# Performance work log

Hardware: AMD Instinct MI355X
Metric: run time of the kernel (lower is better)

Reference implementation:

```python
import jax, jax.numpy as jnp
import numpy as np

N = 100000   # total nodes (batched graphs)
E = 800000   # random edges (self-loops appended -> E+N total)
G = 2000     # number of graphs in batch
H = 4        # heads per GAT layer
D = 64       # hidden_size (per-head out dim)
IN = 64      # in_feats
EXTRA = 8    # extra graph-level feats
HID = H * D  # 256


def setup_inputs() -> dict:
    key = jax.random.key(0)
    ks = jax.random.split(key, 24)
    s = 0.5  # init std used in the torch module
    feats_node = jax.random.normal(ks[0], (N, IN), jnp.float32)
    feats_graph = jax.random.normal(ks[1], (G, EXTRA), jnp.float32)
    # edges + self loops (DGL GATConv requires no zero-in-degree nodes)
    src = jnp.concatenate([jax.random.randint(ks[2], (E,), 0, N), jnp.arange(N)])
    dst = jnp.concatenate([jax.random.randint(ks[3], (E,), 0, N), jnp.arange(N)])
    node_gid = jnp.sort(jax.random.randint(ks[4], (N,), 0, G))
    # GAT layer 1
    W1 = jax.random.normal(ks[5], (IN, HID), jnp.float32) * s
    al1 = jax.random.normal(ks[6], (H, D), jnp.float32) * s
    ar1 = jax.random.normal(ks[7], (H, D), jnp.float32) * s
    b1 = jnp.zeros((HID,), jnp.float32)
    # GAT layer 2
    W2 = jax.random.normal(ks[8], (HID, HID), jnp.float32) * s
    al2 = jax.random.normal(ks[9], (H, D), jnp.float32) * s
    ar2 = jax.random.normal(ks[10], (H, D), jnp.float32) * s
    b2 = jnp.zeros((HID,), jnp.float32)
    # WeightedAverage readout score
    Ws = jax.random.normal(ks[11], (HID, 1), jnp.float32) * s
    bs = jnp.zeros((1,), jnp.float32)
    # MLP: 264 -> 128 -> 64 -> 1 with SELU
    Wm1 = jax.random.normal(ks[12], (HID + EXTRA, 2 * D), jnp.float32) * s
    bm1 = jnp.zeros((2 * D,), jnp.float32)
    Wm2 = jax.random.normal(ks[13], (2 * D, D), jnp.float32) * s
    bm2 = jnp.zeros((D,), jnp.float32)
    Wm3 = jax.random.normal(ks[14], (D, 1), jnp.float32) * s
    bm3 = jnp.zeros((1,), jnp.float32)
    return dict(feats_node=feats_node, feats_graph=feats_graph,
                W1=W1, al1=al1, ar1=ar1, b1=b1,
                W2=W2, al2=al2, ar2=ar2, b2=b2,
                Ws=Ws, bs=bs, Wm1=Wm1, bm1=bm1, Wm2=Wm2, bm2=bm2,
                Wm3=Wm3, bm3=bm3,
                src=src, dst=dst, node_gid=node_gid)


def gat_layer(x, W, al, ar, b, src, dst):
    # DGL GATConv: fc -> per-node attn projections -> edge leaky_relu ->
    # edge softmax over incoming edges -> weighted scatter-sum -> +bias
    f = (x @ W).reshape(N, H, D)                       # [N,H,D]
    el = jnp.einsum('nhd,hd->nh', f, al)               # [N,H]
    er = jnp.einsum('nhd,hd->nh', f, ar)               # [N,H]
    e = jax.nn.leaky_relu(el[src] + er[dst], 0.2)      # [E',H]
    m = jax.ops.segment_max(e, dst, num_segments=N)    # per-dst max
    e = jnp.exp(e - m[dst])
    denom = jax.ops.segment_sum(e, dst, num_segments=N)
    alpha = e / denom[dst]                             # edge softmax [E',H]
    out = jax.ops.segment_sum(alpha[:, :, None] * f[src], dst, num_segments=N)
    return out.reshape(N, HID) + b


def reference(feats_node, feats_graph, W1, al1, ar1, b1, W2, al2, ar2, b2,
              Ws, bs, Wm1, bm1, Wm2, bm2, Wm3, bm3, src, dst, node_gid):
    x = jax.nn.relu(gat_layer(feats_node, W1, al1, ar1, b1, src, dst))
    x = jax.nn.relu(gat_layer(x, W2, al2, ar2, b2, src, dst))
    # weighted-average readout per graph: sum(w*x)/sum(w)
    w = jax.nn.sigmoid(x @ Ws + bs)                    # [N,1]
    num = jax.ops.segment_sum(w * x, node_gid, num_segments=G)
    den = jax.ops.segment_sum(w, node_gid, num_segments=G)
    emb = num / jnp.where(den == 0, 1.0, den)          # [G,HID]
    h = jnp.concatenate([emb, feats_graph], axis=1)    # [G,HID+EXTRA]
    h = jax.nn.selu(h @ Wm1 + bm1)
    h = jax.nn.selu(h @ Wm2 + bm2)
    return h @ Wm3 + bm3                               # [G,1]
```

## Files before the change

### kernel.cpp

```cpp
#include <hip/hip_runtime.h>
#include <hip/hip_bf16.h>
#include <math.h>

#define NN     100000
#define GG     2000
#define HH     4
#define DD     64
#define HID    256
#define INF_   64
#define EXTRA  8

typedef unsigned short u16;
typedef __attribute__((ext_vector_type(8))) short bf16x8;
typedef __attribute__((ext_vector_type(4))) float f32x4;

__device__ __forceinline__ u16 f2bf(float f) {
    unsigned u = __float_as_uint(f);
    return (u16)((u + 0x7fffu + ((u >> 16) & 1u)) >> 16);
}
__device__ __forceinline__ float bf2f(u16 v) {
    return __uint_as_float(((unsigned)v) << 16);
}

__global__ __launch_bounds__(256) void wsplit_kernel(
    const float* __restrict__ W, u16* __restrict__ hi, u16* __restrict__ lo,
    int K, int lgK)
{
    int idx = blockIdx.x * 256 + threadIdx.x;
    if (idx >= 256 * K) return;
    int n = idx >> lgK, k = idx & (K - 1);
    float w = W[k * HID + n];
    u16 h = f2bf(w);
    hi[idx] = h;
    lo[idx] = f2bf(w - bf2f(h));
}

__global__ __launch_bounds__(256) void walprep_kernel(
    const float* __restrict__ W1, const float* __restrict__ al,
    const float* __restrict__ ar, float* __restrict__ wal, float* __restrict__ war)
{
    int tid = threadIdx.x;
    int d = tid >> 2, h = tid & 3;
    const float* wrow = W1 + d * HID + h * DD;
    const float* av = al + h * DD;
    const float* bv = ar + h * DD;
    float s1 = 0.f, s2 = 0.f;
    for (int c = 0; c < DD; ++c) { s1 += wrow[c] * av[c]; s2 += wrow[c] * bv[c]; }
    wal[d * 4 + h] = s1;
    war[d * 4 + h] = s2;
}

__global__ __launch_bounds__(256) void elr1_kernel(
    const float* __restrict__ feats, const float* __restrict__ wal,
    const float* __restrict__ war, float* __restrict__ el, float* __restrict__ er)
{
    int idx = blockIdx.x * 256 + threadIdx.x;
    if (idx >= NN * HH) return;
    int n = idx >> 2, h = idx & 3;
    const float* f = feats + (size_t)n * INF_;
    float s1 = 0.f, s2 = 0.f;
    #pragma unroll 4
    for (int d = 0; d < INF_; d += 4) {
        float4 fv = *reinterpret_cast<const float4*>(f + d);
        s1 += fv.x * wal[(d + 0) * 4 + h] + fv.y * wal[(d + 1) * 4 + h]
            + fv.z * wal[(d + 2) * 4 + h] + fv.w * wal[(d + 3) * 4 + h];
        s2 += fv.x * war[(d + 0) * 4 + h] + fv.y * war[(d + 1) * 4 + h]
            + fv.z * war[(d + 2) * 4 + h] + fv.w * war[(d + 3) * 4 + h];
    }
    el[idx] = s1;
    er[idx] = s2;
}

__device__ __forceinline__ float leaky02(float x) { return x > 0.f ? x : 0.2f * x; }

__global__ __launch_bounds__(256) void edge_softmax_kernel(
    const float* __restrict__ el, const float* __restrict__ er,
    const int* __restrict__ rowptr, const int* __restrict__ colsrc,
    float* __restrict__ w, float* __restrict__ invden)
{
    int idx = blockIdx.x * 256 + threadIdx.x;
    if (idx >= NN * HH) return;
    int t = idx >> 2, h = idx & 3;
    int beg = rowptr[t], end = rowptr[t + 1];
    float ert = er[idx];
    float m = -1e30f;
    for (int i = beg; i < end; ++i) {
        int s = colsrc[i];
        m = fmaxf(m, leaky02(el[s * 4 + h] + ert));
    }
    float den = 0.f;
    for (int i = beg; i < end; ++i) {
        int s = colsrc[i];
        float v = expf(leaky02(el[s * 4 + h] + ert) - m);
        w[(size_t)i * 4 + h] = v;
        den += v;
    }
    invden[idx] = 1.f / den;
}

__global__ __launch_bounds__(256) void aggregate_feats_kernel(
    const float* __restrict__ feats, const float* __restrict__ w,
    const float* __restrict__ invden, const int* __restrict__ rowptr,
    const int* __restrict__ colsrc, u16* __restrict__ Yh, u16* __restrict__ Yl)
{
    int t = blockIdx.x * 4 + (threadIdx.x >> 6);
    int lane = threadIdx.x & 63;
    if (t >= NN) return;
    int beg = rowptr[t], end = rowptr[t + 1];
    float a0 = 0.f, a1 = 0.f, a2 = 0.f, a3 = 0.f;
    float b0 = 0.f, b1 = 0.f, b2 = 0.f, b3 = 0.f;
    int i = beg;
    for (; i + 1 < end; i += 2) {
        int s0 = colsrc[i], s1 = colsrc[i + 1];
        float4 w0 = *reinterpret_cast<const float4*>(w + (size_t)i * 4);
        float4 w1 = *reinterpret_cast<const float4*>(w + (size_t)(i + 1) * 4);
        float f0 = feats[(size_t)s0 * INF_ + lane];
        float f1 = feats[(size_t)s1 * INF_ + lane];
        a0 += w0.x * f0; a1 += w0.y * f0; a2 += w0.z * f0; a3 += w0.w * f0;
        b0 += w1.x * f1; b1 += w1.y * f1; b2 += w1.z * f1; b3 += w1.w * f1;
    }
    if (i < end) {
        int s0 = colsrc[i];
        float4 w0 = *reinterpret_cast<const float4*>(w + (size_t)i * 4);
        float f0 = feats[(size_t)s0 * INF_ + lane];
        a0 += w0.x * f0; a1 += w0.y * f0; a2 += w0.z * f0; a3 += w0.w * f0;
    }
    float4 inv = *reinterpret_cast<const float4*>(invden + (size_t)t * 4);
    float y0 = (a0 + b0) * inv.x;
    float y1 = (a1 + b1) * inv.y;
    float y2 = (a2 + b2) * inv.z;
    float y3 = (a3 + b3) * inv.w;
    u16* yh = Yh + (size_t)t * HID;
    u16* yl = Yl + (size_t)t * HID;
    u16 h0 = f2bf(y0), h1 = f2bf(y1), h2 = f2bf(y2), h3 = f2bf(y3);
    yh[lane] = h0;        yl[lane] = f2bf(y0 - bf2f(h0));
    yh[64 + lane] = h1;   yl[64 + lane] = f2bf(y1 - bf2f(h1));
    yh[128 + lane] = h2;  yl[128 + lane] = f2bf(y2 - bf2f(h2));
    yh[192 + lane] = h3;  yl[192 + lane] = f2bf(y3 - bf2f(h3));
}

__global__ __launch_bounds__(256) void gemm_head_kernel(
    const u16* __restrict__ Yh, const u16* __restrict__ Yl,
    const u16* __restrict__ BThi, const u16* __restrict__ BTlo,
    const float* __restrict__ bias,
    u16* __restrict__ Xh, u16* __restrict__ Xl, int M)
{
    __shared__ __align__(16) u16 Ah[128 * 64];
    __shared__ __align__(16) u16 Al[128 * 64];
    __shared__ __align__(16) u16 Bh[64 * 64];
    __shared__ __align__(16) u16 Bl[64 * 64];
    const int tid  = threadIdx.x;
    const int wave = tid >> 6, lane = tid & 63;
    const int quad = lane >> 4, l15 = lane & 15;
    const int wy = wave >> 1, wx = wave & 1;
    const int head = blockIdx.y;
    const int r0 = blockIdx.x * 128;
    const int cb = head * DD;

    {
        int row = tid >> 1, half = tid & 1;
        int gr = min(r0 + row, M - 1);
        size_t goff = (size_t)gr * HID + cb;
        #pragma unroll
        for (int m = 0; m < 4; ++m) {
            int c = half * 4 + m;
            int cs = c ^ (row & 7);
            *reinterpret_cast<bf16x8*>(&Ah[row * 64 + cs * 8]) =
                *reinterpret_cast<const bf16x8*>(Yh + goff + c * 8);
            *reinterpret_cast<bf16x8*>(&Al[row * 64 + cs * 8]) =
                *reinterpret_cast<const bf16x8*>(Yl + goff + c * 8);
        }
        int d = tid & 63, seg = tid >> 6;
        size_t boff = (size_t)(head * DD + d) * 64;
        #pragma unroll
        for (int m = 0; m < 2; ++m) {
            int c = seg * 2 + m;
            int cs = c ^ (d & 7);
            *reinterpret_cast<bf16x8*>(&Bh[d * 64 + cs * 8]) =
                *reinterpret_cast<const bf16x8*>(BThi + boff + c * 8);
            *reinterpret_cast<bf16x8*>(&Bl[d * 64 + cs * 8]) =
                *reinterpret_cast<const bf16x8*>(BTlo + boff + c * 8);
        }
    }
    __syncthreads();

    f32x4 acc[4][2];
    #pragma unroll
    for (int i = 0; i < 4; ++i)
        #pragma unroll
        for (int j = 0; j < 2; ++j)
            acc[i][j] = (f32x4){0.f, 0.f, 0.f, 0.f};

    #pragma unroll
    for (int k0 = 0; k0 < 64; k0 += 32) {
        bf16x8 afh[4], afl[4], bfh[2], bfl[2];
        #pragma unroll
        for (int i = 0; i < 4; ++i) {
            int Ra = wy * 64 + i * 16 + l15;
            int c = (k0 >> 3) + quad;
            int cs = c ^ (Ra & 7);
            afh[i] = *reinterpret_cast<const bf16x8*>(&Ah[Ra * 64 + cs * 8]);
            afl[i] = *reinterpret_cast<const bf16x8*>(&Al[Ra * 64 + cs * 8]);
        }
        #pragma unroll
        for (int j = 0; j < 2; ++j) {
            int Rb = wx * 32 + j * 16 + l15;
            int c = (k0 >> 3) + quad;
            int cs = c ^ (Rb & 7);
            bfh[j] = *reinterpret_cast<const bf16x8*>(&Bh[Rb * 64 + cs * 8]);
            bfl[j] = *reinterpret_cast<const bf16x8*>(&Bl[Rb * 64 + cs * 8]);
        }
        #pragma unroll
        for (int i = 0; i < 4; ++i)
            #pragma unroll
            for (int j = 0; j < 2; ++j) {
                acc[i][j] = __builtin_amdgcn_mfma_f32_16x16x32_bf16(afh[i], bfh[j], acc[i][j], 0, 0, 0);
                acc[i][j] = __builtin_amdgcn_mfma_f32_16x16x32_bf16(afl[i], bfh[j], acc[i][j], 0, 0, 0);
                acc[i][j] = __builtin_amdgcn_mfma_f32_16x16x32_bf16(afh[i], bfl[j], acc[i][j], 0, 0, 0);
            }
    }

    float bv[2];
    #pragma unroll
    for (int j = 0; j < 2; ++j) bv[j] = bias[cb + wx * 32 + j * 16 + l15];
    #pragma unroll
    for (int i = 0; i < 4; ++i)
        #pragma unroll
        for (int rr = 0; rr < 4; ++rr) {
            int grow = r0 + wy * 64 + i * 16 + quad * 4 + rr;
            if (grow < M) {
                size_t base = (size_t)grow * HID + cb + wx * 32 + l15;
                #pragma unroll
                for (int j = 0; j < 2; ++j) {
                    float x = fmaxf(acc[i][j][rr] + bv[j], 0.f);
                    u16 h = f2bf(x);
                    Xh[base + j * 16] = h;
                    Xl[base + j * 16] = f2bf(x - bf2f(h));
                }
            }
        }
}

__global__ __launch_bounds__(256) void mfma_gemm_kernel(
    const u16* __restrict__ Ahg, const u16* __restrict__ Alg,
    const u16* __restrict__ BThi, const u16* __restrict__ BTlo,
    u16* __restrict__ Cb,
    const float* __restrict__ al, const float* __restrict__ ar,
    float* __restrict__ el, float* __restrict__ er, int M, int K)
{
    __shared__ __align__(16) u16 Ah[128 * 32];
    __shared__ __align__(16) u16 Al[128 * 32];
    __shared__ __align__(16) u16 Bh[128 * 32];
    __shared__ __align__(16) u16 Bl[128 * 32];
    const int tid  = threadIdx.x;
    const int wave = tid >> 6, lane = tid & 63;
    const int quad = lane >> 4, l15 = lane & 15;
    const int wy = wave >> 1, wx = wave & 1;
    const int r0 = blockIdx.x * 128, c0 = blockIdx.y * 128;
    const int sr = tid >> 2, sseg = tid & 3;

    f32x4 acc[4][4];
    #pragma unroll
    for (int i = 0; i < 4; ++i)
        #pragma unroll
        for (int j = 0; j < 4; ++j)
            acc[i][j] = (f32x4){0.f, 0.f, 0.f, 0.f};

    for (int k0 = 0; k0 < K; k0 += 32) {
        #pragma unroll
        for (int half = 0; half < 2; ++half) {
            int r = sr + half * 64;
            int cs = (sseg ^ ((r >> 1) & 3)) * 8;
            int gr = min(r0 + r, M - 1);
            size_t aoff = (size_t)gr * K + k0 + sseg * 8;
            *reinterpret_cast<bf16x8*>(&Ah[r * 32 + cs]) =
                *reinterpret_cast<const bf16x8*>(Ahg + aoff);
            *reinterpret_cast<bf16x8*>(&Al[r * 32 + cs]) =
                *reinterpret_cast<const bf16x8*>(Alg + aoff);
            int gc = c0 + r;
            size_t boff = (size_t)gc * K + k0 + sseg * 8;
            *reinterpret_cast<bf16x8*>(&Bh[r * 32 + cs]) =
                *reinterpret_cast<const bf16x8*>(BThi + boff);
            *reinterpret_cast<bf16x8*>(&Bl[r * 32 + cs]) =
                *reinterpret_cast<const bf16x8*>(BTlo + boff);
        }
        __syncthreads();
        bf16x8 afh[4], afl[4], bfh[4], bfl[4];
        #pragma unroll
        for (int i = 0; i < 4; ++i) {
            int Ra = wy * 64 + i * 16 + l15;
            int off = Ra * 32 + (quad ^ ((Ra >> 1) & 3)) * 8;
            afh[i] = *reinterpret_cast<const bf16x8*>(&Ah[off]);
            afl[i] = *reinterpret_cast<const bf16x8*>(&Al[off]);
        }
        #pragma unroll
        for (int j = 0; j < 4; ++j) {
            int Rb = wx * 64 + j * 16 + l15;
            int off = Rb * 32 + (quad ^ ((Rb >> 1) & 3)) * 8;
            bfh[j] = *reinterpret_cast<const bf16x8*>(&Bh[off]);
            bfl[j] = *reinterpret_cast<const bf16x8*>(&Bl[off]);
        }
        #pragma unroll
        for (int i = 0; i < 4; ++i)
            #pragma unroll
            for (int j = 0; j < 4; ++j) {
                acc[i][j] = __builtin_amdgcn_mfma_f32_16x16x32_bf16(afh[i], bfh[j], acc[i][j], 0, 0, 0);
                acc[i][j] = __builtin_amdgcn_mfma_f32_16x16x32_bf16(afl[i], bfh[j], acc[i][j], 0, 0, 0);
                acc[i][j] = __builtin_amdgcn_mfma_f32_16x16x32_bf16(afh[i], bfl[j], acc[i][j], 0, 0, 0);
            }
        __syncthreads();
    }

    #pragma unroll
    for (int i = 0; i < 4; ++i)
        #pragma unroll
        for (int rr = 0; rr < 4; ++rr) {
            int grow = r0 + wy * 64 + i * 16 + quad * 4 + rr;
            if (grow < M) {
                u16* crow = Cb + (size_t)grow * HID + c0 + wx * 64 + l15;
                #pragma unroll
                for (int j = 0; j < 4; ++j) crow[j * 16] = f2bf(acc[i][j][rr]);
            }
        }

    const int h = blockIdx.y * 2 + wx;
    float alf[4], arf[4];
    #pragma unroll
    for (int j = 0; j < 4; ++j) {
        alf[j] = al[h * DD + j * 16 + l15];
        arf[j] = ar[h * DD + j * 16 + l15];
    }
    #pragma unroll
    for (int i = 0; i < 4; ++i)
        #pragma unroll
        for (int rr = 0; rr < 4; ++rr) {
            float sl = acc[i][0][rr] * alf[0] + acc[i][1][rr] * alf[1]
                     + acc[i][2][rr] * alf[2] + acc[i][3][rr] * alf[3];
            float sr_ = acc[i][0][rr] * arf[0] + acc[i][1][rr] * arf[1]
                      + acc[i][2][rr] * arf[2] + acc[i][3][rr] * arf[3];
            #pragma unroll
            for (int off = 1; off < 16; off <<= 1) {
                sl  += __shfl_xor(sl, off, 64);
                sr_ += __shfl_xor(sr_, off, 64);
            }
            if (l15 == 0) {
                int grow = r0 + wy * 64 + i * 16 + quad * 4 + rr;
                if (grow < M) {
                    el[grow * 4 + h] = sl;
                    er[grow * 4 + h] = sr_;
                }
            }
        }
}

__global__ __launch_bounds__(256) void aggregate_bf16_kernel(
    const u16* __restrict__ F, const float* __restrict__ w,
    const float* __restrict__ invden, const int* __restrict__ rowptr,
    const int* __restrict__ colsrc, const float* __restrict__ bias,
    u16* __restrict__ out)
{
    int t = blockIdx.x * 4 + (threadIdx.x >> 6);
    int lane = threadIdx.x & 63;
    if (t >= NN) return;
    int beg = rowptr[t], end = rowptr[t + 1];
    const int h = lane >> 4;
    float4 acc0 = make_float4(0.f, 0.f, 0.f, 0.f);
    float4 acc1 = make_float4(0.f, 0.f, 0.f, 0.f);
    int i = beg;
    for (; i + 1 < end; i += 2) {
        int s0 = colsrc[i], s1 = colsrc[i + 1];
        float w0 = w[(size_t)i * 4 + h];
        float w1 = w[(size_t)(i + 1) * 4 + h];
        ushort4 f0 = *reinterpret_cast<const ushort4*>(F + (size_t)s0 * HID + 4 * lane);
        ushort4 f1 = *reinterpret_cast<const ushort4*>(F + (size_t)s1 * HID + 4 * lane);
        acc0.x += w0 * bf2f(f0.x); acc0.y += w0 * bf2f(f0.y);
        acc0.z += w0 * bf2f(f0.z); acc0.w += w0 * bf2f(f0.w);
        acc1.x += w1 * bf2f(f1.x); acc1.y += w1 * bf2f(f1.y);
        acc1.z += w1 * bf2f(f1.z); acc1.w += w1 * bf2f(f1.w);
    }
    if (i < end) {
        int s0 = colsrc[i];
        float w0 = w[(size_t)i * 4 + h];
        ushort4 f0 = *reinterpret_cast<const ushort4*>(F + (size_t)s0 * HID + 4 * lane);
        acc0.x += w0 * bf2f(f0.x); acc0.y += w0 * bf2f(f0.y);
        acc0.z += w0 * bf2f(f0.z); acc0.w += w0 * bf2f(f0.w);
    }
    float inv = invden[t * 4 + h];
    float4 bv = *reinterpret_cast<const float4*>(bias + 4 * lane);
    ushort4 r;
    r.x = f2bf(fmaxf((acc0.x + acc1.x) * inv + bv.x, 0.f));
    r.y = f2bf(fmaxf((acc0.y + acc1.y) * inv + bv.y, 0.f));
    r.z = f2bf(fmaxf((acc0.z + acc1.z) * inv + bv.z, 0.f));
    r.w = f2bf(fmaxf((acc0.w + acc1.w) * inv + bv.w, 0.f));
    *reinterpret_cast<ushort4*>(out + (size_t)t * HID + 4 * lane) = r;
}

__global__ __launch_bounds__(256) void readout_kernel(
    const u16* __restrict__ X, const float* __restrict__ Ws,
    const float* __restrict__ bs, const int* __restrict__ gptr,
    float* __restrict__ emb)
{
    int g = blockIdx.x * 4 + (threadIdx.x >> 6);
    int lane = threadIdx.x & 63;
    if (g >= GG) return;
    int beg = gptr[g], end = gptr[g + 1];
    float4 wv = *reinterpret_cast<const float4*>(Ws + 4 * lane);
    float b = bs[0];
    float4 acc = make_float4(0.f, 0.f, 0.f, 0.f);
    float wsum = 0.f;
    for (int n = beg; n < end; ++n) {
        ushort4 xv = *reinterpret_cast<const ushort4*>(X + (size_t)n * HID + 4 * lane);
        float x0 = bf2f(xv.x), x1 = bf2f(xv.y), x2 = bf2f(xv.z), x3 = bf2f(xv.w);
        float p = x0 * wv.x + x1 * wv.y + x2 * wv.z + x3 * wv.w;
        #pragma unroll
        for (int off = 32; off; off >>= 1) p += __shfl_xor(p, off, 64);
        float w = 1.f / (1.f + expf(-(p + b)));
        wsum += w;
        acc.x += w * x0; acc.y += w * x1; acc.z += w * x2; acc.w += w * x3;
    }
    float inv = (wsum == 0.f) ? 1.f : wsum;
    float4 e;
    e.x = acc.x / inv; e.y = acc.y / inv; e.z = acc.z / inv; e.w = acc.w / inv;
    *reinterpret_cast<float4*>(emb + (size_t)g * HID + 4 * lane) = e;
}

__device__ __forceinline__ float selu_f(float x)
{
    const float scale = 1.0507009873554805f, alpha = 1.6732632423543772f;
    return scale * (x > 0.f ? x : alpha * expm1f(x));
}

__global__ __launch_bounds__(128) void mlp_kernel(
    const float* __restrict__ emb, const float* __restrict__ fg,
    const float* __restrict__ Wm1, const float* __restrict__ bm1,
    const float* __restrict__ Wm2, const float* __restrict__ bm2,
    const float* __restrict__ Wm3, const float* __restrict__ bm3,
    float* __restrict__ out)
{
    int g = blockIdx.x;
    __shared__ float h[HID + EXTRA];
    __shared__ float h1[128];
    __shared__ float h2[64];
    int tid = threadIdx.x;
    h[tid] = emb[(size_t)g * HID + tid];
    h[128 + tid] = emb[(size_t)g * HID + 128 + tid];
    if (tid < EXTRA) h[HID + tid] = fg[(size_t)g * EXTRA + tid];
    __syncthreads();
    float acc = bm1[tid];
    for (int i = 0; i < HID + EXTRA; ++i) acc += h[i] * Wm1[i * 128 + tid];
    h1[tid] = selu_f(acc);
    __syncthreads();
    if (tid < 64) {
        float acc2 = bm2[tid];
        for (int i = 0; i < 128; ++i) acc2 += h1[i] * Wm2[i * 64 + tid];
        h2[tid] = selu_f(acc2);
    }
    __syncthreads();
    if (tid < 64) {
        float p = h2[tid] * Wm3[tid];
        #pragma unroll
        for (int off = 32; off; off >>= 1) p += __shfl_xor(p, off, 64);
        if (tid == 0) out[g] = p + bm3[0];
    }
}

__global__ void count_dst_kernel(const int* __restrict__ dst, int* __restrict__ cnt, int E)
{
    int e = blockIdx.x * 256 + threadIdx.x;
    if (e < E) atomicAdd(&cnt[dst[e]], 1);
}
__global__ void fill_csr_kernel(const int* __restrict__ src, const int* __restrict__ dst,
                                int* __restrict__ cursor, int* __restrict__ colsrc, int E)
{
    int e = blockIdx.x * 256 + threadIdx.x;
    if (e < E) {
        int p = atomicAdd(&cursor[dst[e]], 1);
        colsrc[p] = src[e];
    }
}

__global__ void gid_ranges_kernel(const int* __restrict__ gid, int* __restrict__ gptr, int n)
{
    int i = blockIdx.x * 256 + threadIdx.x;
    if (i >= n) return;
    int cur = gid[i];
    int prev = (i == 0) ? -1 : gid[i - 1];
    for (int g = prev + 1; g <= cur; ++g) gptr[g] = i;
    if (i == n - 1)
        for (int g = cur + 1; g <= GG; ++g) gptr[g] = n;
}

__global__ __launch_bounds__(256) void scan_blocks_kernel(
    const int* __restrict__ in, int n, int* __restrict__ out, int* __restrict__ partials)
{
    __shared__ int lds[256];
    int tid = threadIdx.x;
    int base = blockIdx.x * 1024 + tid * 4;
    int v0 = (base + 0 < n) ? in[base + 0] : 0;
    int v1 = (base + 1 < n) ? in[base + 1] : 0;
    int v2 = (base + 2 < n) ? in[base + 2] : 0;
    int v3 = (base + 3 < n) ? in[base + 3] : 0;
    int s = v0 + v1 + v2 + v3;
    lds[tid] = s;
    __syncthreads();
    for (int off = 1; off < 256; off <<= 1) {
        int t = (tid >= off) ? lds[tid - off] : 0;
        __syncthreads();
        lds[tid] += t;
        __syncthreads();
    }
    int excl = lds[tid] - s;
    if (base + 0 < n) out[base + 0] = excl;
    if (base + 1 < n) out[base + 1] = excl + v0;
    if (base + 2 < n) out[base + 2] = excl + v0 + v1;
    if (base + 3 < n) out[base + 3] = excl + v0 + v1 + v2;
    if (tid == 255) partials[blockIdx.x] = lds[255];
}

__global__ __launch_bounds__(256) void scan_partials_kernel(int* partials, int nb)
{
    __shared__ int lds[256];
    int tid = threadIdx.x;
    int v = (tid < nb) ? partials[tid] : 0;
    lds[tid] = v;
    __syncthreads();
    for (int off = 1; off < 256; off <<= 1) {
        int t = (tid >= off) ? lds[tid - off] : 0;
        __syncthreads();
        lds[tid] += t;
        __syncthreads();
    }
    int excl = lds[tid] - v;
    if (tid < nb) partials[tid] = excl;
}

__global__ void add_offsets_kernel(int* __restrict__ out, const int* __restrict__ partials, int n)
{
    int i = blockIdx.x * 256 + threadIdx.x;
    if (i < n) out[i] += partials[i >> 10];
}

extern "C" void kernel_launch(void* const* d_in, const int* in_sizes, int n_in,
                              void* d_out, int out_size, void* d_ws, size_t ws_size,
                              hipStream_t stream)
{
    const float* feats_node  = (const float*)d_in[0];
    const float* feats_graph = (const float*)d_in[1];
    const float* W1  = (const float*)d_in[2];
    const float* al1 = (const float*)d_in[3];
    const float* ar1 = (const float*)d_in[4];
    const float* b1  = (const float*)d_in[5];
    const float* W2  = (const float*)d_in[6];
    const float* al2 = (const float*)d_in[7];
    const float* ar2 = (const float*)d_in[8];
    const float* b2  = (const float*)d_in[9];
    const float* Ws  = (const float*)d_in[10];
    const float* bs  = (const float*)d_in[11];
    const float* Wm1 = (const float*)d_in[12];
    const float* bm1 = (const float*)d_in[13];
    const float* Wm2 = (const float*)d_in[14];
    const float* bm2 = (const float*)d_in[15];
    const float* Wm3 = (const float*)d_in[16];
    const float* bm3 = (const float*)d_in[17];
    const int* src = (const int*)d_in[18];
    const int* dst = (const int*)d_in[19];
    const int* gid = (const int*)d_in[20];
    float* out = (float*)d_out;
    const int E = in_sizes[18];

    char* p = (char*)d_ws;
    auto alloc = [&](size_t bytes) {
        char* r = p;
        p += (bytes + 255) & ~(size_t)255;
        return r;
    };
    u16*   Yh     = (u16*)alloc((size_t)NN * HID * 2);
    u16*   Yl     = (u16*)alloc((size_t)NN * HID * 2);
    u16*   Xh     = (u16*)alloc((size_t)NN * HID * 2);
    u16*   Xl     = (u16*)alloc((size_t)NN * HID * 2);
    float* el     = (float*)alloc((size_t)NN * HH * 4);
    float* er     = (float*)alloc((size_t)NN * HH * 4);
    float* wbuf   = (float*)alloc((size_t)E * HH * 4);
    float* invden = (float*)alloc((size_t)NN * HH * 4);
    int*   cnt    = (int*)alloc((size_t)(NN + 1) * 4);
    int*   rowptr = (int*)alloc((size_t)(NN + 1) * 4);
    int*   colsrc = (int*)alloc((size_t)E * 4);
    int*   gptr   = (int*)alloc((size_t)(GG + 1) * 4);
    int*   parts  = (int*)alloc(1024 * 4);
    float* emb    = (float*)alloc((size_t)GG * HID * 4);
    u16*   BT1h   = (u16*)alloc((size_t)HID * INF_ * 2);
    u16*   BT1l   = (u16*)alloc((size_t)HID * INF_ * 2);
    u16*   BT2h   = (u16*)alloc((size_t)HID * HID * 2);
    u16*   BT2l   = (u16*)alloc((size_t)HID * HID * 2);
    float* wal1   = (float*)alloc(INF_ * HH * 4);
    float* war1   = (float*)alloc(INF_ * HH * 4);
    u16*   Fbf2   = Yh;
    u16*   Xbf2   = Xh;

    hipMemsetAsync(cnt, 0, (size_t)(NN + 1) * 4, stream);
    count_dst_kernel<<<(E + 255) / 256, 256, 0, stream>>>(dst, cnt, E);
    {
        int n = NN + 1, nb = (n + 1023) / 1024;
        scan_blocks_kernel<<<nb, 256, 0, stream>>>(cnt, n, rowptr, parts);
        scan_partials_kernel<<<1, 256, 0, stream>>>(parts, nb);
        add_offsets_kernel<<<(n + 255) / 256, 256, 0, stream>>>(rowptr, parts, n);
    }
    hipMemcpyAsync(cnt, rowptr, (size_t)(NN + 1) * 4, hipMemcpyDeviceToDevice, stream);
    fill_csr_kernel<<<(E + 255) / 256, 256, 0, stream>>>(src, dst, cnt, colsrc, E);

    gid_ranges_kernel<<<(NN + 255) / 256, 256, 0, stream>>>(gid, gptr, NN);

    wsplit_kernel<<<(HID * INF_ + 255) / 256, 256, 0, stream>>>(W1, BT1h, BT1l, INF_, 6);
    wsplit_kernel<<<(HID * HID + 255) / 256, 256, 0, stream>>>(W2, BT2h, BT2l, HID, 8);
    walprep_kernel<<<1, 256, 0, stream>>>(W1, al1, ar1, wal1, war1);

    const int nh_blocks = (NN * HH + 255) / 256;

    elr1_kernel<<<nh_blocks, 256, 0, stream>>>(feats_node, wal1, war1, el, er);
    edge_softmax_kernel<<<nh_blocks, 256, 0, stream>>>(el, er, rowptr, colsrc, wbuf, invden);
    aggregate_feats_kernel<<<(NN + 3) / 4, 256, 0, stream>>>(feats_node, wbuf, invden,
                                                             rowptr, colsrc, Yh, Yl);
    {
        dim3 hgrid((NN + 127) / 128, HH);
        gemm_head_kernel<<<hgrid, 256, 0, stream>>>(Yh, Yl, BT1h, BT1l, b1, Xh, Xl, NN);
    }

    dim3 ggrid((NN + 127) / 128, HID / 128);
    mfma_gemm_kernel<<<ggrid, 256, 0, stream>>>(
        Xh, Xl, BT2h, BT2l, Fbf2, al2, ar2, el, er, NN, HID);
    edge_softmax_kernel<<<nh_blocks, 256, 0, stream>>>(el, er, rowptr, colsrc, wbuf, invden);
    aggregate_bf16_kernel<<<(NN + 3) / 4, 256, 0, stream>>>(Fbf2, wbuf, invden, rowptr, colsrc,
                                                            b2, Xbf2);

    readout_kernel<<<(GG + 3) / 4, 256, 0, stream>>>(Xbf2, Ws, bs, gptr, emb);
    mlp_kernel<<<GG, 128, 0, stream>>>(emb, feats_graph, Wm1, bm1, Wm2, bm2, Wm3, bm3, out);
}
```

Before: 600.7 us.

## Pre-tile weight fragments in MFMA order and load B directly from global

The weight split kernel now writes hi/lo bf16 weights in a fragment-major layout matching the MFMA 16x8 B-operand shape. Both GEMM kernels drop their shared-memory B tiles and instead load B fragments straight from global memory, relying on cache hits since the weights are small and shared across blocks. This cuts LDS traffic and footprint, which may raise occupancy. The cost is more global or L2 loads per wave in the inner loop.

New measurement: 609.6 us. Within noise of the previous version (+1.5%).

```diff
diff --git a/kernel.cpp b/kernel.cpp
--- a/kernel.cpp
+++ b/kernel.cpp
@@ -31,8 +31,9 @@
     int n = idx >> lgK, k = idx & (K - 1);
     float w = W[k * HID + n];
     u16 h = f2bf(w);
-    hi[idx] = h;
-    lo[idx] = f2bf(w - bf2f(h));
+    int off = (((n >> 4) * (K >> 3) + (k >> 3)) << 7) + ((n & 15) << 3) + (k & 7);
+    hi[off] = h;
+    lo[off] = f2bf(w - bf2f(h));
 }
 
 __global__ __launch_bounds__(256) void walprep_kernel(
@@ -147,8 +148,6 @@
 {
     __shared__ __align__(16) u16 Ah[128 * 64];
     __shared__ __align__(16) u16 Al[128 * 64];
-    __shared__ __align__(16) u16 Bh[64 * 64];
-    __shared__ __align__(16) u16 Bl[64 * 64];
     const int tid  = threadIdx.x;
     const int wave = tid >> 6, lane = tid & 63;
     const int quad = lane >> 4, l15 = lane & 15;
@@ -170,17 +169,6 @@
             *reinterpret_cast<bf16x8*>(&Al[row * 64 + cs * 8]) =
                 *reinterpret_cast<const bf16x8*>(Yl + goff + c * 8);
         }
-        int d = tid & 63, seg = tid >> 6;
-        size_t boff = (size_t)(head * DD + d) * 64;
-        #pragma unroll
-        for (int m = 0; m < 2; ++m) {
-            int c = seg * 2 + m;
-            int cs = c ^ (d & 7);
-            *reinterpret_cast<bf16x8*>(&Bh[d * 64 + cs * 8]) =
-                *reinterpret_cast<const bf16x8*>(BThi + boff + c * 8);
-            *reinterpret_cast<bf16x8*>(&Bl[d * 64 + cs * 8]) =
-                *reinterpret_cast<const bf16x8*>(BTlo + boff + c * 8);
-        }
     }
     __syncthreads();
 
@@ -194,6 +182,14 @@
     #pragma unroll
     for (int k0 = 0; k0 < 64; k0 += 32) {
         bf16x8 afh[4], afl[4], bfh[2], bfl[2];
+        #pragma unroll
+        for (int j = 0; j < 2; ++j) {
+            int nb = head * 4 + wx * 2 + j;
+            int kc = (k0 >> 3) + quad;
+            size_t off = ((size_t)(nb * 8 + kc) << 7) + (l15 << 3);
+            bfh[j] = *reinterpret_cast<const bf16x8*>(BThi + off);
+            bfl[j] = *reinterpret_cast<const bf16x8*>(BTlo + off);
+        }
         #pragma unroll
         for (int i = 0; i < 4; ++i) {
             int Ra = wy * 64 + i * 16 + l15;
@@ -201,14 +197,6 @@
             int cs = c ^ (Ra & 7);
             afh[i] = *reinterpret_cast<const bf16x8*>(&Ah[Ra * 64 + cs * 8]);
             afl[i] = *reinterpret_cast<const bf16x8*>(&Al[Ra * 64 + cs * 8]);
-        }
-        #pragma unroll
-        for (int j = 0; j < 2; ++j) {
-            int Rb = wx * 32 + j * 16 + l15;
-            int c = (k0 >> 3) + quad;
-            int cs = c ^ (Rb & 7);
-            bfh[j] = *reinterpret_cast<const bf16x8*>(&Bh[Rb * 64 + cs * 8]);
-            bfl[j] = *reinterpret_cast<const bf16x8*>(&Bl[Rb * 64 + cs * 8]);
         }
         #pragma unroll
         for (int i = 0; i < 4; ++i)
@@ -250,8 +238,6 @@
 {
     __shared__ __align__(16) u16 Ah[128 * 32];
     __shared__ __align__(16) u16 Al[128 * 32];
-    __shared__ __align__(16) u16 Bh[128 * 32];
-    __shared__ __align__(16) u16 Bl[128 * 32];
     const int tid  = threadIdx.x;
     const int wave = tid >> 6, lane = tid & 63;
     const int quad = lane >> 4, l15 = lane & 15;
@@ -266,6 +252,7 @@
         for (int j = 0; j < 4; ++j)
             acc[i][j] = (f32x4){0.f, 0.f, 0.f, 0.f};
 
+    const int Kc = K >> 3;
     for (int k0 = 0; k0 < K; k0 += 32) {
         #pragma unroll
         for (int half = 0; half < 2; ++half) {
@@ -277,28 +264,23 @@
                 *reinterpret_cast<const bf16x8*>(Ahg + aoff);
             *reinterpret_cast<bf16x8*>(&Al[r * 32 + cs]) =
                 *reinterpret_cast<const bf16x8*>(Alg + aoff);
-            int gc = c0 + r;
-            size_t boff = (size_t)gc * K + k0 + sseg * 8;
-            *reinterpret_cast<bf16x8*>(&Bh[r * 32 + cs]) =
-                *reinterpret_cast<const bf16x8*>(BThi + boff);
-            *reinterpret_cast<bf16x8*>(&Bl[r * 32 + cs]) =
-                *reinterpret_cast<const bf16x8*>(BTlo + boff);
         }
         __syncthreads();
         bf16x8 afh[4], afl[4], bfh[4], bfl[4];
+        #pragma unroll
+        for (int j = 0; j < 4; ++j) {
+            int nb = (c0 + wx * 64 + j * 16) >> 4;
+            int kc = (k0 >> 3) + quad;
+            size_t off = ((size_t)(nb * Kc + kc) << 7) + (l15 << 3);
+            bfh[j] = *reinterpret_cast<const bf16x8*>(BThi + off);
+            bfl[j] = *reinterpret_cast<const bf16x8*>(BTlo + off);
+        }
         #pragma unroll
         for (int i = 0; i < 4; ++i) {
             int Ra = wy * 64 + i * 16 + l15;
             int off = Ra * 32 + (quad ^ ((Ra >> 1) & 3)) * 8;
             afh[i] = *reinterpret_cast<const bf16x8*>(&Ah[off]);
             afl[i] = *reinterpret_cast<const bf16x8*>(&Al[off]);
-        }
-        #pragma unroll
-        for (int j = 0; j < 4; ++j) {
-            int Rb = wx * 64 + j * 16 + l15;
-            int off = Rb * 32 + (quad ^ ((Rb >> 1) & 3)) * 8;
-            bfh[j] = *reinterpret_cast<const bf16x8*>(&Bh[off]);
-            bfl[j] = *reinterpret_cast<const bf16x8*>(&Bl[off]);
         }
         #pragma unroll
         for (int i = 0; i < 4; ++i)
```
